# Kernel optimization log

Measured on AMD Instinct MI355X. Metric: run time of the kernel, lower is better.

## Reference

```python
import jax, jax.numpy as jnp
import numpy as np

COST_CLASS, COST_BBOX, COST_GIOU = 1.0, 5.0, 2.0


def box_cxcywh_to_xyxy(b):
    cx, cy, w, h = jnp.split(b, 4, axis=-1)
    return jnp.concatenate([cx - 0.5 * w, cy - 0.5 * h, cx + 0.5 * w, cy + 0.5 * h], axis=-1)


def generalized_box_iou(a, b):
    # a: [N,4] xyxy, b: [M,4] xyxy -> [N,M]
    area_a = (a[:, 2] - a[:, 0]) * (a[:, 3] - a[:, 1])
    area_b = (b[:, 2] - b[:, 0]) * (b[:, 3] - b[:, 1])
    lt = jnp.maximum(a[:, None, :2], b[None, :, :2])
    rb = jnp.minimum(a[:, None, 2:], b[None, :, 2:])
    wh = jnp.clip(rb - lt, 0.0)
    inter = wh[..., 0] * wh[..., 1]
    union = area_a[:, None] + area_b[None, :] - inter
    iou = inter / union
    lt2 = jnp.minimum(a[:, None, :2], b[None, :, :2])
    rb2 = jnp.maximum(a[:, None, 2:], b[None, :, 2:])
    wh2 = jnp.clip(rb2 - lt2, 0.0)
    encl = wh2[..., 0] * wh2[..., 1]
    return iou - (encl - union) / encl


@jax.jit
def _cost_matrix(pred_logits, pred_boxes, tgt_labels, tgt_boxes):
    bs, Q, _ = pred_logits.shape
    out_prob = jax.nn.softmax(pred_logits.reshape(bs * Q, -1), axis=-1)   # [bs*Q, C]
    out_bbox = pred_boxes.reshape(bs * Q, 4)                              # [bs*Q, 4]
    tgt_ids = tgt_labels.reshape(-1)                                      # [bs*T]
    tgt_bb = tgt_boxes.reshape(-1, 4)                                     # [bs*T, 4]
    cost_class = 1.0 - out_prob[:, tgt_ids]                               # [bs*Q, bs*T]
    cost_bbox = jnp.sum(jnp.abs(out_bbox[:, None, :] - tgt_bb[None, :, :]), axis=-1)  # L1 cdist
    cost_giou = 1.0 - generalized_box_iou(box_cxcywh_to_xyxy(out_bbox), box_cxcywh_to_xyxy(tgt_bb))
    C = COST_BBOX * cost_bbox + COST_CLASS * cost_class + COST_GIOU * cost_giou
    return C.reshape(bs, Q, -1)                                           # [bs, Q, bs*T]


def _lsa(cost):
    # Hungarian (shortest augmenting path / Jonker-Volgenant), cost: [n, m], n <= m.
    # Returns, for each row i, the assigned column (globally optimal assignment).
    n, m = cost.shape
    INF = 1e18
    u = np.zeros(n + 1)
    v = np.zeros(m + 1)
    p = np.zeros(m + 1, dtype=np.int64)    # p[j] = row matched to column j (1-indexed, 0 = free)
    way = np.zeros(m + 1, dtype=np.int64)
    for i in range(1, n + 1):
        p[0] = i
        j0 = 0
        minv = np.full(m + 1, INF)
        used = np.zeros(m + 1, dtype=bool)
        while True:
            used[j0] = True
            i0 = p[j0]
            cur = cost[i0 - 1] - u[i0] - v[1:]
            mask = ~used[1:]
            upd = mask & (cur < minv[1:])
            minv[1:] = np.where(upd, cur, minv[1:])
            way[1:] = np.where(upd, j0, way[1:])
            cand = np.where(mask, minv[1:], INF)
            j1 = int(np.argmin(cand)) + 1
            delta = cand[j1 - 1]
            u[p[used]] += delta
            v[used] -= delta
            minv[1:] = np.where(mask, minv[1:] - delta, minv[1:])
            j0 = j1
            if p[j0] == 0:
                break
        while j0:
            j1 = way[j0]
            p[j0] = p[j1]
            j0 = j1
    rows = np.zeros(n, dtype=np.int64)
    for j in range(1, m + 1):
        if p[j] > 0:
            rows[p[j] - 1] = j - 1
    return rows


def setup_inputs() -> dict:
    key = jax.random.key(0)
    k1, k2, k3, k4 = jax.random.split(key, 4)
    bs, Q, C, T = 32, 900, 91, 30
    return {
        'pred_logits': jax.random.normal(k1, (bs, Q, C), dtype=jnp.float32),
        'pred_boxes': jax.random.uniform(k2, (bs, Q, 4), dtype=jnp.float32),
        'tgt_labels': jax.random.randint(k3, (bs, T), 0, C),
        'tgt_boxes': jax.random.uniform(k4, (bs, T, 4), dtype=jnp.float32),
    }


def reference(pred_logits, pred_boxes, tgt_labels, tgt_boxes):
    C3 = _cost_matrix(pred_logits, pred_boxes, tgt_labels, tgt_boxes)  # [bs, Q, bs*T]
    bs, Q, _ = C3.shape
    T = tgt_labels.shape[1]
    C_np = np.asarray(jax.device_get(C3), dtype=np.float64)
    pred_idx = np.zeros((bs, T), dtype=np.int64)
    tgt_idx = np.zeros((bs, T), dtype=np.int64)
    for i in range(bs):
        c = C_np[i, :, i * T:(i + 1) * T]        # per-image block [Q, T] (== split-by-sizes)
        preds = _lsa(c.T)                        # for each target, matched prediction
        order = np.argsort(preds, kind='stable') # scipy returns row indices sorted ascending
        pred_idx[i] = preds[order]
        tgt_idx[i] = np.arange(T, dtype=np.int64)[order]
    return C3, jnp.asarray(pred_idx), jnp.asarray(tgt_idx)
```

## Files before the change

kernel.cpp:

```cpp
#include <hip/hip_runtime.h>
#include <hip/hip_bf16.h>
#include <math.h>

#define BS 32
#define NQ 900
#define NC 91
#define NT 30
#define NJ (BS*NT)
#define C3_SZ ((size_t)BS*NQ*NJ)
#define NROWS (BS*NQ)

#define LT 960
#define LWAVES (LT/64)
#define NCOSTBLK 224
#define MAXROWS 132

__device__ __forceinline__ float fast_rcp(float x) { return __builtin_amdgcn_rcpf(x); }

struct SharedLSA {
    float  cst[NT * NQ];
    float  mx[NQ];
    float  rs[NQ];
    double u[NT + 1];
    int    p[NQ + 1];
    int    way[NQ + 1];
    double red_v[LWAVES];
    int    red_i[LWAVES];
    int    rows[NT];
    int    tl[NT];
    float4 tbox[NT];
    float  rminv[NT];
    int    rminc[NT];
    int    aflag[NT + 1];
};
struct SharedCost {
    float  prob[MAXROWS][NC];
    float4 pbx[MAXROWS];
};

__device__ __forceinline__ float cost_elem(
    float pcx, float pcy, float pw, float ph,
    float px0, float py0, float px1, float py1, float area_a,
    float pr,
    float tcx, float tcy, float tw, float th,
    float tx0, float ty0, float tx1, float ty1, float area_b)
{
    float cost_bbox = fabsf(pcx - tcx) + fabsf(pcy - tcy) + fabsf(pw - tw) + fabsf(ph - th);
    float ix0 = fmaxf(px0, tx0), iy0 = fmaxf(py0, ty0);
    float ix1 = fminf(px1, tx1), iy1 = fminf(py1, ty1);
    float inter = fmaxf(ix1 - ix0, 0.f) * fmaxf(iy1 - iy0, 0.f);
    float uni = area_a + area_b - inter;
    float iou = inter * fast_rcp(uni);
    float ex0 = fminf(px0, tx0), ey0 = fminf(py0, ty0);
    float ex1 = fmaxf(px1, tx1), ey1 = fmaxf(py1, ty1);
    float encl = fmaxf(ex1 - ex0, 0.f) * fmaxf(ey1 - ey0, 0.f);
    float giou = iou - (encl - uni) * fast_rcp(encl);
    return 5.0f * cost_bbox - pr - 2.0f * giou + 3.0f;
}

__device__ __forceinline__ void softmax_row(const float* __restrict__ lrow, int lane,
                                            float* out_mx, float* out_rs)
{
    float a = (lane < NC)      ? lrow[lane]      : -1e30f;
    float c = (lane + 64 < NC) ? lrow[lane + 64] : -1e30f;
    float m = fmaxf(a, c);
    for (int off = 32; off; off >>= 1) m = fmaxf(m, __shfl_xor(m, off));
    float ea = (lane < NC)      ? __expf(a - m) : 0.f;
    float ec = (lane + 64 < NC) ? __expf(c - m) : 0.f;
    float s = ea + ec;
    for (int off = 32; off; off >>= 1) s += __shfl_xor(s, off);
    if (lane == 0) { *out_mx = m; *out_rs = fast_rcp(s); }
}

__device__ __forceinline__ void softmax_prob_row(const float* __restrict__ lrow, int lane,
                                                 float* __restrict__ prob)
{
    float a = (lane < NC)      ? lrow[lane]      : -1e30f;
    float c = (lane + 64 < NC) ? lrow[lane + 64] : -1e30f;
    float m = fmaxf(a, c);
    for (int off = 32; off; off >>= 1) m = fmaxf(m, __shfl_xor(m, off));
    float ea = (lane < NC)      ? __expf(a - m) : 0.f;
    float ec = (lane + 64 < NC) ? __expf(c - m) : 0.f;
    float s = ea + ec;
    for (int off = 32; off; off >>= 1) s += __shfl_xor(s, off);
    float rs = fast_rcp(s);
    if (lane < NC)      prob[lane]      = ea * rs;
    if (lane + 64 < NC) prob[lane + 64] = ec * rs;
}

__global__ __launch_bounds__(LT) void fused_kernel(
    const float* __restrict__ logits,
    const float* __restrict__ pboxes,
    const int*   __restrict__ tlabels,
    const float* __restrict__ tboxes,
    float* __restrict__ out,
    float* __restrict__ outp,
    float* __restrict__ outt)
{
    __shared__ union { SharedLSA l; SharedCost c; } sm;
    const int t = threadIdx.x;
    const int wv = t >> 6;
    const int lane = t & 63;

    if (blockIdx.x < BS) {
        const int b = blockIdx.x;
        const float* lg  = logits + (size_t)b * NQ * NC;
        const float* pbx = pboxes + (size_t)b * NQ * 4;

        for (int q = wv; q < NQ; q += LWAVES)
            softmax_row(lg + (size_t)q * NC, lane, &sm.l.mx[q], &sm.l.rs[q]);
        if (t < NT) {
            sm.l.tl[t] = tlabels[b * NT + t];
            sm.l.tbox[t] = ((const float4*)tboxes)[b * NT + t];
        }
        for (int j = t; j <= NQ; j += LT) { sm.l.p[j] = 0; sm.l.way[j] = 0; }
        __syncthreads();

        for (int e = t; e < NT * NQ; e += LT) {
            int q = e / NT;
            int r = e - q * NT;
            float4 pb = ((const float4*)pbx)[q];
            float pcx = pb.x, pcy = pb.y, pw = pb.z, ph = pb.w;
            float px0 = pcx - 0.5f*pw, py0 = pcy - 0.5f*ph;
            float px1 = pcx + 0.5f*pw, py1 = pcy + 0.5f*ph;
            float area_a = pw * ph;
            int   lbl = sm.l.tl[r];
            float pr = __expf(lg[(size_t)q * NC + lbl] - sm.l.mx[q]) * sm.l.rs[q];
            float4 tb = sm.l.tbox[r];
            float tcx = tb.x, tcy = tb.y, tw = tb.z, th = tb.w;
            float tx0 = tcx - 0.5f*tw, ty0 = tcy - 0.5f*th;
            float tx1 = tcx + 0.5f*tw, ty1 = tcy + 0.5f*th;
            float area_b = tw * th;
            sm.l.cst[r * NQ + q] = cost_elem(pcx, pcy, pw, ph, px0, py0, px1, py1, area_a,
                                             pr, tcx, tcy, tw, th, tx0, ty0, tx1, ty1, area_b);
        }
        __syncthreads();

        for (int r = wv; r < NT; r += LWAVES) {
            float bv = 1e30f; int bi = 1 << 20;
            for (int j = lane; j < NQ; j += 64) {
                float v = sm.l.cst[r * NQ + j];
                if (v < bv) { bv = v; bi = j; }
            }
            for (int off = 32; off; off >>= 1) {
                float ov = __shfl_xor(bv, off);
                int   oi = __shfl_xor(bi, off);
                if (ov < bv || (ov == bv && oi < bi)) { bv = ov; bi = oi; }
            }
            if (lane == 0) { sm.l.rminv[r] = bv; sm.l.rminc[r] = bi + 1; }
        }
        __syncthreads();
        if (t == 0) {
            for (int r = 1; r <= NT; ++r) {
                sm.l.u[r] = (double)sm.l.rminv[r - 1];
                int c = sm.l.rminc[r - 1];
                if (sm.l.p[c] == 0) { sm.l.p[c] = r; sm.l.aflag[r] = 1; }
                else                 sm.l.aflag[r] = 0;
            }
        }
        double v_t = 0.0;
        __syncthreads();

        for (int i = 1; i <= NT; ++i) {
            if (sm.l.aflag[i]) continue;
            double minv_t = 1e18;
            bool used_t = (t == 0);
            int p_t = (t == 0) ? i : ((t <= NQ) ? sm.l.p[t] : 0);
            int i0 = i, j0 = 0, j1f = 0;
            for (;;) {
                double u_i0 = sm.l.u[i0];
                double cand; int ci;
                if (t >= 1 && t <= NQ && !used_t) {
                    double cur = ((double)sm.l.cst[(i0 - 1) * NQ + (t - 1)] - u_i0) - v_t;
                    if (cur < minv_t) { minv_t = cur; sm.l.way[t] = j0; }
                    cand = minv_t; ci = t;
                } else { cand = 1e18; ci = 1 << 20; }
                for (int off = 32; off; off >>= 1) {
                    double ov = __shfl_xor(cand, off);
                    int    oi = __shfl_xor(ci, off);
                    if (ov < cand || (ov == cand && oi < ci)) { cand = ov; ci = oi; }
                }
                if (lane == 0) { sm.l.red_v[wv] = cand; sm.l.red_i[wv] = ci; }
                __syncthreads();
                double rv; int ri;
                if (lane < LWAVES) { rv = sm.l.red_v[lane]; ri = sm.l.red_i[lane]; }
                else               { rv = 1e18;             ri = 1 << 20; }
                for (int off = 8; off; off >>= 1) {
                    double ov = __shfl_xor(rv, off);
                    int    oi = __shfl_xor(ri, off);
                    if (ov < rv || (ov == rv && oi < ri)) { rv = ov; ri = oi; }
                }
                double delta = __shfl(rv, 0);
                int    j1    = __shfl(ri, 0);
                if (used_t) { v_t -= delta; sm.l.u[p_t] += delta; }
                else if (t >= 1 && t <= NQ) minv_t -= delta;
                if (t == j1) { used_t = true; p_t = sm.l.p[j1]; }
                int pj1 = sm.l.p[j1];
                __syncthreads();
                if (pj1 == 0) { j1f = j1; break; }
                i0 = pj1; j0 = j1;
            }
            if (t == 0) {
                int j0w = j1f;
                while (j0w) {
                    int jp = sm.l.way[j0w];
                    sm.l.p[j0w] = (jp == 0) ? i : sm.l.p[jp];
                    j0w = jp;
                }
            }
            __syncthreads();
        }
        if (t >= 1 && t <= NQ && sm.l.p[t] > 0) sm.l.rows[sm.l.p[t] - 1] = t - 1;
        __syncthreads();
        if (t == 0) {
            int pr[NT], tg[NT];
            for (int r = 0; r < NT; ++r) { pr[r] = sm.l.rows[r]; tg[r] = r; }
            for (int a = 1; a < NT; ++a) {
                int kp = pr[a], kt = tg[a]; int bnd = a - 1;
                while (bnd >= 0 && pr[bnd] > kp) { pr[bnd+1] = pr[bnd]; tg[bnd+1] = tg[bnd]; --bnd; }
                pr[bnd+1] = kp; tg[bnd+1] = kt;
            }
            for (int k = 0; k < NT; ++k) {
                outp[b*NT + k] = (float)pr[k];
                outt[b*NT + k] = (float)tg[k];
            }
        }
    } else {
        const int cb = blockIdx.x - BS;
        const int r0 = (int)(((long long)cb * NROWS) / NCOSTBLK);
        const int r1 = (int)(((long long)(cb + 1) * NROWS) / NCOSTBLK);
        const int nrows = r1 - r0;

        for (int rr = wv; rr < nrows; rr += LWAVES)
            softmax_prob_row(logits + (size_t)(r0 + rr) * NC, lane, sm.c.prob[rr]);
        for (int rr = t; rr < nrows; rr += LT)
            sm.c.pbx[rr] = ((const float4*)pboxes)[r0 + rr];

        const int   lbl = tlabels[t];
        const float4 tb = ((const float4*)tboxes)[t];
        const float tcx = tb.x, tcy = tb.y, tw = tb.z, th = tb.w;
        const float tx0 = tcx - 0.5f*tw, ty0 = tcy - 0.5f*th;
        const float tx1 = tcx + 0.5f*tw, ty1 = tcy + 0.5f*th;
        const float area_b = tw * th;
        __syncthreads();

        float* op = out + (size_t)r0 * NJ + t;
        #pragma unroll 2
        for (int rr = 0; rr < nrows; ++rr) {
            float pr = sm.c.prob[rr][lbl];
            float4 pb = sm.c.pbx[rr];
            float pcx = pb.x, pcy = pb.y, pw = pb.z, ph = pb.w;
            float px0 = pcx - 0.5f*pw, py0 = pcy - 0.5f*ph;
            float px1 = pcx + 0.5f*pw, py1 = pcy + 0.5f*ph;
            float area_a = pw * ph;
            float v = cost_elem(pcx, pcy, pw, ph, px0, py0, px1, py1, area_a,
                                pr, tcx, tcy, tw, th, tx0, ty0, tx1, ty1, area_b);
            __builtin_nontemporal_store(v, op);
            op += NJ;
        }
    }
}

extern "C" void kernel_launch(void* const* d_in, const int* in_sizes, int n_in,
                              void* d_out, int out_size, void* d_ws, size_t ws_size,
                              hipStream_t stream) {
    const float* logits  = (const float*)d_in[0];
    const float* pboxes  = (const float*)d_in[1];
    const int*   tlabels = (const int*)d_in[2];
    const float* tboxes  = (const float*)d_in[3];
    float* out = (float*)d_out;

    fused_kernel<<<BS + NCOSTBLK, LT, 0, stream>>>(
        logits, pboxes, tlabels, tboxes,
        out, out + C3_SZ, out + C3_SZ + (size_t)BS * NT);
}
```

Baseline: 221.3 us.

## Split into cooperative grid: all blocks compute cost matrix, then 32 run LSA

Replaces the heterogeneous launch, where 32 blocks recomputed their per-image cost blocks and ran the Hungarian solver alongside 224 cost blocks, with a cooperative kernel. All 256 blocks first compute the full cost matrix, a grid-wide sync follows, and then the first 32 blocks read their diagonal block back from global memory and run the assignment. This removes the redundant softmax and cost recomputation in the LSA blocks and spreads the cost work over every block. In exchange the serial LSA can no longer overlap with cost generation, and a grid barrier plus a global reload are added. Bounds guards are also added to the augmenting loop.

Result: slower. 366.0 us (+65.4%).

```diff
diff --git a/kernel.cpp b/kernel.cpp
--- a/kernel.cpp
+++ b/kernel.cpp
@@ -1,6 +1,8 @@
 #include <hip/hip_runtime.h>
-#include <hip/hip_bf16.h>
+#include <hip/hip_cooperative_groups.h>
 #include <math.h>
+
+namespace cg = cooperative_groups;
 
 #define BS 32
 #define NQ 900
@@ -12,23 +14,19 @@
 
 #define LT 960
 #define LWAVES (LT/64)
-#define NCOSTBLK 224
-#define MAXROWS 132
+#define NBLK 256
+#define MAXROWS 113
 
 __device__ __forceinline__ float fast_rcp(float x) { return __builtin_amdgcn_rcpf(x); }
 
 struct SharedLSA {
     float  cst[NT * NQ];
-    float  mx[NQ];
-    float  rs[NQ];
     double u[NT + 1];
     int    p[NQ + 1];
     int    way[NQ + 1];
     double red_v[LWAVES];
     int    red_i[LWAVES];
     int    rows[NT];
-    int    tl[NT];
-    float4 tbox[NT];
     float  rminv[NT];
     int    rminc[NT];
     int    aflag[NT + 1];
@@ -58,20 +56,6 @@
     return 5.0f * cost_bbox - pr - 2.0f * giou + 3.0f;
 }
 
-__device__ __forceinline__ void softmax_row(const float* __restrict__ lrow, int lane,
-                                            float* out_mx, float* out_rs)
-{
-    float a = (lane < NC)      ? lrow[lane]      : -1e30f;
-    float c = (lane + 64 < NC) ? lrow[lane + 64] : -1e30f;
-    float m = fmaxf(a, c);
-    for (int off = 32; off; off >>= 1) m = fmaxf(m, __shfl_xor(m, off));
-    float ea = (lane < NC)      ? __expf(a - m) : 0.f;
-    float ec = (lane + 64 < NC) ? __expf(c - m) : 0.f;
-    float s = ea + ec;
-    for (int off = 32; off; off >>= 1) s += __shfl_xor(s, off);
-    if (lane == 0) { *out_mx = m; *out_rs = fast_rcp(s); }
-}
-
 __device__ __forceinline__ void softmax_prob_row(const float* __restrict__ lrow, int lane,
                                                  float* __restrict__ prob)
 {
@@ -88,7 +72,7 @@
     if (lane + 64 < NC) prob[lane + 64] = ec * rs;
 }
 
-__global__ __launch_bounds__(LT) void fused_kernel(
+__global__ __launch_bounds__(LT) void coop_kernel(
     const float* __restrict__ logits,
     const float* __restrict__ pboxes,
     const int*   __restrict__ tlabels,
@@ -102,133 +86,10 @@
     const int wv = t >> 6;
     const int lane = t & 63;
 
-    if (blockIdx.x < BS) {
-        const int b = blockIdx.x;
-        const float* lg  = logits + (size_t)b * NQ * NC;
-        const float* pbx = pboxes + (size_t)b * NQ * 4;
-
-        for (int q = wv; q < NQ; q += LWAVES)
-            softmax_row(lg + (size_t)q * NC, lane, &sm.l.mx[q], &sm.l.rs[q]);
-        if (t < NT) {
-            sm.l.tl[t] = tlabels[b * NT + t];
-            sm.l.tbox[t] = ((const float4*)tboxes)[b * NT + t];
-        }
-        for (int j = t; j <= NQ; j += LT) { sm.l.p[j] = 0; sm.l.way[j] = 0; }
-        __syncthreads();
-
-        for (int e = t; e < NT * NQ; e += LT) {
-            int q = e / NT;
-            int r = e - q * NT;
-            float4 pb = ((const float4*)pbx)[q];
-            float pcx = pb.x, pcy = pb.y, pw = pb.z, ph = pb.w;
-            float px0 = pcx - 0.5f*pw, py0 = pcy - 0.5f*ph;
-            float px1 = pcx + 0.5f*pw, py1 = pcy + 0.5f*ph;
-            float area_a = pw * ph;
-            int   lbl = sm.l.tl[r];
-            float pr = __expf(lg[(size_t)q * NC + lbl] - sm.l.mx[q]) * sm.l.rs[q];
-            float4 tb = sm.l.tbox[r];
-            float tcx = tb.x, tcy = tb.y, tw = tb.z, th = tb.w;
-            float tx0 = tcx - 0.5f*tw, ty0 = tcy - 0.5f*th;
-            float tx1 = tcx + 0.5f*tw, ty1 = tcy + 0.5f*th;
-            float area_b = tw * th;
-            sm.l.cst[r * NQ + q] = cost_elem(pcx, pcy, pw, ph, px0, py0, px1, py1, area_a,
-                                             pr, tcx, tcy, tw, th, tx0, ty0, tx1, ty1, area_b);
-        }
-        __syncthreads();
-
-        for (int r = wv; r < NT; r += LWAVES) {
-            float bv = 1e30f; int bi = 1 << 20;
-            for (int j = lane; j < NQ; j += 64) {
-                float v = sm.l.cst[r * NQ + j];
-                if (v < bv) { bv = v; bi = j; }
-            }
-            for (int off = 32; off; off >>= 1) {
-                float ov = __shfl_xor(bv, off);
-                int   oi = __shfl_xor(bi, off);
-                if (ov < bv || (ov == bv && oi < bi)) { bv = ov; bi = oi; }
-            }
-            if (lane == 0) { sm.l.rminv[r] = bv; sm.l.rminc[r] = bi + 1; }
-        }
-        __syncthreads();
-        if (t == 0) {
-            for (int r = 1; r <= NT; ++r) {
-                sm.l.u[r] = (double)sm.l.rminv[r - 1];
-                int c = sm.l.rminc[r - 1];
-                if (sm.l.p[c] == 0) { sm.l.p[c] = r; sm.l.aflag[r] = 1; }
-                else                 sm.l.aflag[r] = 0;
-            }
-        }
-        double v_t = 0.0;
-        __syncthreads();
-
-        for (int i = 1; i <= NT; ++i) {
-            if (sm.l.aflag[i]) continue;
-            double minv_t = 1e18;
-            bool used_t = (t == 0);
-            int p_t = (t == 0) ? i : ((t <= NQ) ? sm.l.p[t] : 0);
-            int i0 = i, j0 = 0, j1f = 0;
-            for (;;) {
-                double u_i0 = sm.l.u[i0];
-                double cand; int ci;
-                if (t >= 1 && t <= NQ && !used_t) {
-                    double cur = ((double)sm.l.cst[(i0 - 1) * NQ + (t - 1)] - u_i0) - v_t;
-                    if (cur < minv_t) { minv_t = cur; sm.l.way[t] = j0; }
-                    cand = minv_t; ci = t;
-                } else { cand = 1e18; ci = 1 << 20; }
-                for (int off = 32; off; off >>= 1) {
-                    double ov = __shfl_xor(cand, off);
-                    int    oi = __shfl_xor(ci, off);
-                    if (ov < cand || (ov == cand && oi < ci)) { cand = ov; ci = oi; }
-                }
-                if (lane == 0) { sm.l.red_v[wv] = cand; sm.l.red_i[wv] = ci; }
-                __syncthreads();
-                double rv; int ri;
-                if (lane < LWAVES) { rv = sm.l.red_v[lane]; ri = sm.l.red_i[lane]; }
-                else               { rv = 1e18;             ri = 1 << 20; }
-                for (int off = 8; off; off >>= 1) {
-                    double ov = __shfl_xor(rv, off);
-                    int    oi = __shfl_xor(ri, off);
-                    if (ov < rv || (ov == rv && oi < ri)) { rv = ov; ri = oi; }
-                }
-                double delta = __shfl(rv, 0);
-                int    j1    = __shfl(ri, 0);
-                if (used_t) { v_t -= delta; sm.l.u[p_t] += delta; }
-                else if (t >= 1 && t <= NQ) minv_t -= delta;
-                if (t == j1) { used_t = true; p_t = sm.l.p[j1]; }
-                int pj1 = sm.l.p[j1];
-                __syncthreads();
-                if (pj1 == 0) { j1f = j1; break; }
-                i0 = pj1; j0 = j1;
-            }
-            if (t == 0) {
-                int j0w = j1f;
-                while (j0w) {
-                    int jp = sm.l.way[j0w];
-                    sm.l.p[j0w] = (jp == 0) ? i : sm.l.p[jp];
-                    j0w = jp;
-                }
-            }
-            __syncthreads();
-        }
-        if (t >= 1 && t <= NQ && sm.l.p[t] > 0) sm.l.rows[sm.l.p[t] - 1] = t - 1;
-        __syncthreads();
-        if (t == 0) {
-            int pr[NT], tg[NT];
-            for (int r = 0; r < NT; ++r) { pr[r] = sm.l.rows[r]; tg[r] = r; }
-            for (int a = 1; a < NT; ++a) {
-                int kp = pr[a], kt = tg[a]; int bnd = a - 1;
-                while (bnd >= 0 && pr[bnd] > kp) { pr[bnd+1] = pr[bnd]; tg[bnd+1] = tg[bnd]; --bnd; }
-                pr[bnd+1] = kp; tg[bnd+1] = kt;
-            }
-            for (int k = 0; k < NT; ++k) {
-                outp[b*NT + k] = (float)pr[k];
-                outt[b*NT + k] = (float)tg[k];
-            }
-        }
-    } else {
-        const int cb = blockIdx.x - BS;
-        const int r0 = (int)(((long long)cb * NROWS) / NCOSTBLK);
-        const int r1 = (int)(((long long)(cb + 1) * NROWS) / NCOSTBLK);
+    {
+        const int cb = blockIdx.x;
+        const int r0 = (int)(((long long)cb * NROWS) / NBLK);
+        const int r1 = (int)(((long long)(cb + 1) * NROWS) / NBLK);
         const int nrows = r1 - r0;
 
         for (int rr = wv; rr < nrows; rr += LWAVES)
@@ -259,6 +120,115 @@
             op += NJ;
         }
     }
+
+    __threadfence();
+    cg::this_grid().sync();
+    if (blockIdx.x >= BS) return;
+    __threadfence();
+
+    const int b = blockIdx.x;
+
+    for (int j = t; j <= NQ; j += LT) { sm.l.p[j] = 0; sm.l.way[j] = 0; }
+
+    const float* src = out + (size_t)b * NQ * NJ + (size_t)b * NT;
+    for (int e = t; e < NT * NQ; e += LT) {
+        int q = e / NT;
+        int r = e - q * NT;
+        sm.l.cst[r * NQ + q] = src[(size_t)q * NJ + r];
+    }
+    __syncthreads();
+
+    for (int r = wv; r < NT; r += LWAVES) {
+        float bv = 1e30f; int bi = 1 << 20;
+        for (int j = lane; j < NQ; j += 64) {
+            float v = sm.l.cst[r * NQ + j];
+            if (v < bv) { bv = v; bi = j; }
+        }
+        for (int off = 32; off; off >>= 1) {
+            float ov = __shfl_xor(bv, off);
+            int   oi = __shfl_xor(bi, off);
+            if (ov < bv || (ov == bv && oi < bi)) { bv = ov; bi = oi; }
+        }
+        if (lane == 0) { sm.l.rminv[r] = bv; sm.l.rminc[r] = bi + 1; }
+    }
+    __syncthreads();
+    if (t == 0) {
+        for (int r = 1; r <= NT; ++r) {
+            sm.l.u[r] = (double)sm.l.rminv[r - 1];
+            int c = sm.l.rminc[r - 1];
+            if (c >= 1 && c <= NQ && sm.l.p[c] == 0) { sm.l.p[c] = r; sm.l.aflag[r] = 1; }
+            else                                       sm.l.aflag[r] = 0;
+        }
+    }
+    double v_t = 0.0;
+    __syncthreads();
+
+    for (int i = 1; i <= NT; ++i) {
+        if (sm.l.aflag[i]) continue;
+        double minv_t = 1e18;
+        bool used_t = (t == 0);
+        int p_t = (t == 0) ? i : ((t <= NQ) ? sm.l.p[t] : 0);
+        int i0 = i, j0 = 0, j1f = 0;
+        for (int iter = 0; iter < NQ + 8; ++iter) {
+            double u_i0 = sm.l.u[i0];
+            double cand; int ci;
+            if (t >= 1 && t <= NQ && !used_t) {
+                double cur = ((double)sm.l.cst[(i0 - 1) * NQ + (t - 1)] - u_i0) - v_t;
+                if (cur < minv_t) { minv_t = cur; sm.l.way[t] = j0; }
+                cand = minv_t; ci = t;
+            } else { cand = 1e18; ci = 1 << 20; }
+            for (int off = 32; off; off >>= 1) {
+                double ov = __shfl_xor(cand, off);
+                int    oi = __shfl_xor(ci, off);
+                if (ov < cand || (ov == cand && oi < ci)) { cand = ov; ci = oi; }
+            }
+            if (lane == 0) { sm.l.red_v[wv] = cand; sm.l.red_i[wv] = ci; }
+            __syncthreads();
+            double rv; int ri;
+            if (lane < LWAVES) { rv = sm.l.red_v[lane]; ri = sm.l.red_i[lane]; }
+            else               { rv = 1e18;             ri = 1 << 20; }
+            for (int off = 8; off; off >>= 1) {
+                double ov = __shfl_xor(rv, off);
+                int    oi = __shfl_xor(ri, off);
+                if (ov < rv || (ov == rv && oi < ri)) { rv = ov; ri = oi; }
+            }
+            double delta = __shfl(rv, 0);
+            int    j1    = __shfl(ri, 0);
+            int    j1c   = (j1 >= 1 && j1 <= NQ) ? j1 : 0;
+            if (used_t) { v_t -= delta; sm.l.u[p_t] += delta; }
+            else if (t >= 1 && t <= NQ) minv_t -= delta;
+            if (t == j1c && j1c) { used_t = true; p_t = sm.l.p[j1c]; }
+            int pj1 = sm.l.p[j1c];
+            __syncthreads();
+            if (pj1 == 0 || j1c == 0) { j1f = j1c; break; }
+            i0 = pj1; j0 = j1c;
+        }
+        if (t == 0) {
+            int j0w = j1f;
+            int guard = NQ + 1;
+            while (j0w && guard--) {
+                int jp = sm.l.way[j0w];
+                sm.l.p[j0w] = (jp == 0) ? i : sm.l.p[jp];
+                j0w = jp;
+            }
+        }
+        __syncthreads();
+    }
+    if (t >= 1 && t <= NQ && sm.l.p[t] > 0) sm.l.rows[sm.l.p[t] - 1] = t - 1;
+    __syncthreads();
+    if (t == 0) {
+        int pr[NT], tg[NT];
+        for (int r = 0; r < NT; ++r) { pr[r] = sm.l.rows[r]; tg[r] = r; }
+        for (int a = 1; a < NT; ++a) {
+            int kp = pr[a], kt = tg[a]; int bnd = a - 1;
+            while (bnd >= 0 && pr[bnd] > kp) { pr[bnd+1] = pr[bnd]; tg[bnd+1] = tg[bnd]; --bnd; }
+            pr[bnd+1] = kp; tg[bnd+1] = kt;
+        }
+        for (int k = 0; k < NT; ++k) {
+            outp[b*NT + k] = (float)pr[k];
+            outt[b*NT + k] = (float)tg[k];
+        }
+    }
 }
 
 extern "C" void kernel_launch(void* const* d_in, const int* in_sizes, int n_in,
@@ -268,9 +238,12 @@
     const float* pboxes  = (const float*)d_in[1];
     const int*   tlabels = (const int*)d_in[2];
     const float* tboxes  = (const float*)d_in[3];
-    float* out = (float*)d_out;
-
-    fused_kernel<<<BS + NCOSTBLK, LT, 0, stream>>>(
-        logits, pboxes, tlabels, tboxes,
-        out, out + C3_SZ, out + C3_SZ + (size_t)BS * NT);
-}
+    float* out  = (float*)d_out;
+    float* outp = out + C3_SZ;
+    float* outt = outp + (size_t)BS * NT;
+
+    void* args[] = { (void*)&logits, (void*)&pboxes, (void*)&tlabels, (void*)&tboxes,
+                     (void*)&out, (void*)&outp, (void*)&outt };
+    hipLaunchCooperativeKernel(reinterpret_cast<const void*>(&coop_kernel),
+                               dim3(NBLK), dim3(LT), args, 0, stream);
+}
```

## Fuse softmax into LSA cost build; parallelize init and output sort across a wave

Applied to the files above, without the earlier changes.

The LSA blocks now compute each row's softmax and its 30 per-target costs in one wave pass. The probability for each label is taken with a lane shuffle, so the separate max and reciprocal-sum smem arrays and the second global read of the logits are gone. The serial single-thread initial assignment and insertion sort are replaced by wave-parallel versions: conflict resolution by shuffles and a rank-based sort. This shortens the serial critical path of the LSA blocks, which likely dominate kernel time. In exchange, only 30 of 64 lanes are active during the cost computation.

Result: faster. 184.4 us (-16.7%).

```diff
diff --git a/kernel.cpp b/kernel.cpp
--- a/kernel.cpp
+++ b/kernel.cpp
@@ -1,5 +1,4 @@
 #include <hip/hip_runtime.h>
-#include <hip/hip_bf16.h>
 #include <math.h>
 
 #define BS 32
@@ -19,8 +18,6 @@
 
 struct SharedLSA {
     float  cst[NT * NQ];
-    float  mx[NQ];
-    float  rs[NQ];
     double u[NT + 1];
     int    p[NQ + 1];
     int    way[NQ + 1];
@@ -58,20 +55,6 @@
     return 5.0f * cost_bbox - pr - 2.0f * giou + 3.0f;
 }
 
-__device__ __forceinline__ void softmax_row(const float* __restrict__ lrow, int lane,
-                                            float* out_mx, float* out_rs)
-{
-    float a = (lane < NC)      ? lrow[lane]      : -1e30f;
-    float c = (lane + 64 < NC) ? lrow[lane + 64] : -1e30f;
-    float m = fmaxf(a, c);
-    for (int off = 32; off; off >>= 1) m = fmaxf(m, __shfl_xor(m, off));
-    float ea = (lane < NC)      ? __expf(a - m) : 0.f;
-    float ec = (lane + 64 < NC) ? __expf(c - m) : 0.f;
-    float s = ea + ec;
-    for (int off = 32; off; off >>= 1) s += __shfl_xor(s, off);
-    if (lane == 0) { *out_mx = m; *out_rs = fast_rcp(s); }
-}
-
 __device__ __forceinline__ void softmax_prob_row(const float* __restrict__ lrow, int lane,
                                                  float* __restrict__ prob)
 {
@@ -107,8 +90,6 @@
         const float* lg  = logits + (size_t)b * NQ * NC;
         const float* pbx = pboxes + (size_t)b * NQ * 4;
 
-        for (int q = wv; q < NQ; q += LWAVES)
-            softmax_row(lg + (size_t)q * NC, lane, &sm.l.mx[q], &sm.l.rs[q]);
         if (t < NT) {
             sm.l.tl[t] = tlabels[b * NT + t];
             sm.l.tbox[t] = ((const float4*)tboxes)[b * NT + t];
@@ -116,23 +97,37 @@
         for (int j = t; j <= NQ; j += LT) { sm.l.p[j] = 0; sm.l.way[j] = 0; }
         __syncthreads();
 
-        for (int e = t; e < NT * NQ; e += LT) {
-            int q = e / NT;
-            int r = e - q * NT;
-            float4 pb = ((const float4*)pbx)[q];
-            float pcx = pb.x, pcy = pb.y, pw = pb.z, ph = pb.w;
-            float px0 = pcx - 0.5f*pw, py0 = pcy - 0.5f*ph;
-            float px1 = pcx + 0.5f*pw, py1 = pcy + 0.5f*ph;
-            float area_a = pw * ph;
-            int   lbl = sm.l.tl[r];
-            float pr = __expf(lg[(size_t)q * NC + lbl] - sm.l.mx[q]) * sm.l.rs[q];
-            float4 tb = sm.l.tbox[r];
-            float tcx = tb.x, tcy = tb.y, tw = tb.z, th = tb.w;
-            float tx0 = tcx - 0.5f*tw, ty0 = tcy - 0.5f*th;
-            float tx1 = tcx + 0.5f*tw, ty1 = tcy + 0.5f*th;
-            float area_b = tw * th;
-            sm.l.cst[r * NQ + q] = cost_elem(pcx, pcy, pw, ph, px0, py0, px1, py1, area_a,
-                                             pr, tcx, tcy, tw, th, tx0, ty0, tx1, ty1, area_b);
+        for (int q = wv; q < NQ; q += LWAVES) {
+            const float* lrow = lg + (size_t)q * NC;
+            float a = (lane < NC)      ? lrow[lane]      : -1e30f;
+            float c = (lane + 64 < NC) ? lrow[lane + 64] : -1e30f;
+            float m = fmaxf(a, c);
+            for (int off = 32; off; off >>= 1) m = fmaxf(m, __shfl_xor(m, off));
+            float ea = (lane < NC)      ? __expf(a - m) : 0.f;
+            float ec = (lane + 64 < NC) ? __expf(c - m) : 0.f;
+            float s = ea + ec;
+            for (int off = 32; off; off >>= 1) s += __shfl_xor(s, off);
+            float rs = fast_rcp(s);
+
+            int lbl = sm.l.tl[lane < NT ? lane : 0];
+            float pa = __shfl(ea, lbl & 63);
+            float pc = __shfl(ec, lbl & 63);
+            if (lane < NT) {
+                float pr = ((lbl < 64) ? pa : pc) * rs;
+                float4 pb = ((const float4*)pbx)[q];
+                float pcx = pb.x, pcy = pb.y, pw = pb.z, ph = pb.w;
+                float px0 = pcx - 0.5f*pw, py0 = pcy - 0.5f*ph;
+                float px1 = pcx + 0.5f*pw, py1 = pcy + 0.5f*ph;
+                float area_a = pw * ph;
+                float4 tb = sm.l.tbox[lane];
+                float tcx = tb.x, tcy = tb.y, tw = tb.z, th = tb.w;
+                float tx0 = tcx - 0.5f*tw, ty0 = tcy - 0.5f*th;
+                float tx1 = tcx + 0.5f*tw, ty1 = tcy + 0.5f*th;
+                float area_b = tw * th;
+                sm.l.cst[lane * NQ + q] =
+                    cost_elem(pcx, pcy, pw, ph, px0, py0, px1, py1, area_a,
+                              pr, tcx, tcy, tw, th, tx0, ty0, tx1, ty1, area_b);
+            }
         }
         __syncthreads();
 
@@ -150,12 +145,19 @@
             if (lane == 0) { sm.l.rminv[r] = bv; sm.l.rminc[r] = bi + 1; }
         }
         __syncthreads();
-        if (t == 0) {
-            for (int r = 1; r <= NT; ++r) {
-                sm.l.u[r] = (double)sm.l.rminv[r - 1];
-                int c = sm.l.rminc[r - 1];
-                if (sm.l.p[c] == 0) { sm.l.p[c] = r; sm.l.aflag[r] = 1; }
-                else                 sm.l.aflag[r] = 0;
+
+        if (wv == 0) {
+            int r = lane;
+            int myc = (r < NT) ? sm.l.rminc[r] : -1;
+            bool win = (r < NT);
+            for (int j = 0; j < NT; ++j) {
+                int cj = __shfl(myc, j);
+                if (j < r && cj == myc) win = false;
+            }
+            if (r < NT) {
+                sm.l.u[r + 1] = (double)sm.l.rminv[r];
+                sm.l.aflag[r + 1] = win ? 1 : 0;
+                if (win) sm.l.p[myc] = r + 1;
             }
         }
         double v_t = 0.0;
@@ -212,17 +214,18 @@
         }
         if (t >= 1 && t <= NQ && sm.l.p[t] > 0) sm.l.rows[sm.l.p[t] - 1] = t - 1;
         __syncthreads();
-        if (t == 0) {
-            int pr[NT], tg[NT];
-            for (int r = 0; r < NT; ++r) { pr[r] = sm.l.rows[r]; tg[r] = r; }
-            for (int a = 1; a < NT; ++a) {
-                int kp = pr[a], kt = tg[a]; int bnd = a - 1;
-                while (bnd >= 0 && pr[bnd] > kp) { pr[bnd+1] = pr[bnd]; tg[bnd+1] = tg[bnd]; --bnd; }
-                pr[bnd+1] = kp; tg[bnd+1] = kt;
-            }
-            for (int k = 0; k < NT; ++k) {
-                outp[b*NT + k] = (float)pr[k];
-                outt[b*NT + k] = (float)tg[k];
+
+        if (wv == 0) {
+            int k = lane;
+            int key = (k < NT) ? sm.l.rows[k] : 0x7fffffff;
+            int rank = 0;
+            for (int j = 0; j < NT; ++j) {
+                int kj = __shfl(key, j);
+                if (kj < key) ++rank;
+            }
+            if (k < NT) {
+                outp[b * NT + rank] = (float)key;
+                outt[b * NT + rank] = (float)k;
             }
         }
     } else {
```
